# Optimization experiments

Measured on AMD Instinct MI355X. Metric: run time of the kernel, lower is better.

## Reference

```python
import jax, jax.numpy as jnp
import numpy as np

B, T, D, H, HD, I = 256, 1, 2048, 16, 128, 5504
EPS = 1e-6
ROPE_THETA = 10000.0


def setup_inputs() -> dict:
    key = jax.random.key(0)
    ks = jax.random.split(key, 20)
    W = 0.02  # weight init scale
    hidden_states = jax.random.normal(ks[0], (B, T, D), jnp.float32)
    # RoPE tables for each batch element at a distinct decode position
    pos = jnp.arange(B, dtype=jnp.float32) % 4096.0
    inv_freq = 1.0 / (ROPE_THETA ** (jnp.arange(0, HD, 2, dtype=jnp.float32) / HD))
    ang = pos[:, None] * inv_freq[None, :]                      # [B, HD/2]
    emb = jnp.concatenate([ang, ang], axis=-1)                  # [B, HD]
    cos = jnp.cos(emb)[:, None, :]                              # [B, 1, HD]
    sin = jnp.sin(emb)[:, None, :]
    n = lambda k, s: jax.random.normal(k, s, jnp.float32) * W
    return {
        'hidden_states': hidden_states, 'cos': cos, 'sin': sin,
        'router_w': n(ks[1], (D,)), 'router_b': jnp.zeros((1,), jnp.float32),
        'ln1_w': jnp.ones((D,), jnp.float32), 'ln2_w': jnp.ones((D,), jnp.float32),
        'wq': n(ks[2], (D, D)), 'bq': jnp.zeros((D,), jnp.float32),
        'wk': n(ks[3], (D, D)), 'bk': jnp.zeros((D,), jnp.float32),
        'wv': n(ks[4], (D, D)), 'bv': jnp.zeros((D,), jnp.float32),
        'wo': n(ks[5], (D, D)),
        'w_gate': n(ks[6], (D, I)), 'w_up': n(ks[7], (D, I)), 'w_down': n(ks[8], (I, D)),
        'k_sel': 128,
    }


def _rms(x, w):
    v = jnp.mean(jnp.square(x), axis=-1, keepdims=True)
    return x * jax.lax.rsqrt(v + EPS) * w


def _rotate_half(x):
    x1, x2 = jnp.split(x, 2, axis=-1)
    return jnp.concatenate([-x2, x1], axis=-1)


def _decoder_layer(x, cs, sn, ln1_w, ln2_w, wq, bq, wk, bk, wv, bv, wo, w_gate, w_up, w_down):
    # x: [k, T, D]; cs/sn: [k, T, HD]
    k = x.shape[0]
    h = _rms(x, ln1_w)
    q = (h @ wq + bq).reshape(k, T, H, HD).transpose(0, 2, 1, 3)  # [k,H,T,HD]
    kk = (h @ wk + bk).reshape(k, T, H, HD).transpose(0, 2, 1, 3)
    v = (h @ wv + bv).reshape(k, T, H, HD).transpose(0, 2, 1, 3)
    c = cs[:, None, :, :]  # [k,1,T,HD]
    s = sn[:, None, :, :]
    q = q * c + _rotate_half(q) * s
    kk = kk * c + _rotate_half(kk) * s
    att = jnp.einsum('bhqd,bhkd->bhqk', q, kk) * (HD ** -0.5)
    p = jax.nn.softmax(att, axis=-1)  # T==1: trivial causal mask
    o = jnp.einsum('bhqk,bhkd->bhqd', p, v).transpose(0, 2, 1, 3).reshape(k, T, D) @ wo
    x = x + o
    h2 = _rms(x, ln2_w)
    mlp = (jax.nn.silu(h2 @ w_gate) * (h2 @ w_up)) @ w_down
    return x + mlp


def reference(hidden_states, cos, sin, router_w, router_b, ln1_w, ln2_w,
              wq, bq, wk, bk, wv, bv, wo, w_gate, w_up, w_down, k_sel):
    # causal router: linear D->1 scores per batch row (T==1 decode step)
    scores = hidden_states[:, 0, :] @ router_w + router_b[0]   # [B]
    probs = jax.nn.sigmoid(scores)
    _, sel_idx = jax.lax.top_k(probs, k_sel)                   # [k]
    x_sel = hidden_states[sel_idx]                             # gather [k,T,D]
    cs, sn = cos[sel_idx], sin[sel_idx]                        # [k,T,HD]
    x_out = _decoder_layer(x_sel, cs, sn, ln1_w, ln2_w, wq, bq, wk, bk,
                           wv, bv, wo, w_gate, w_up, w_down)
    return hidden_states.at[sel_idx].set(x_out)                # scatter back
```

## Files before the change

### kernel.cpp

```cpp
#include <hip/hip_runtime.h>
#include <hip/hip_bf16.h>
#include <stdint.h>


#define D_ 2048
#define I_ 5504
#define NROWS 256
#define KSEL 128

typedef __attribute__((ext_vector_type(8))) short short8;
typedef __attribute__((ext_vector_type(4))) float floatx4;

__device__ __forceinline__ unsigned short f2bf(float f) {
  union { float f; unsigned int u; } v; v.f = f;
  unsigned int r = (v.u + 0x7FFFu + ((v.u >> 16) & 1u)) >> 16;
  return (unsigned short)r;
}

__device__ __forceinline__ unsigned int pk2(float lo, float hi) {
  __hip_bfloat162 h = __float22bfloat162_rn(float2{lo, hi});
  unsigned int u; __builtin_memcpy(&u, &h, 4); return u;
}

__global__ void k_router(const float* __restrict__ hid, const float* __restrict__ rw,
                         const float* __restrict__ rb, float* __restrict__ scores) {
  int b = blockIdx.x, t = threadIdx.x;
  const float* x = hid + (size_t)b * D_;
  float s = 0.f;
  for (int i = t; i < D_; i += 256) s += x[i] * rw[i];
  for (int o = 32; o; o >>= 1) s += __shfl_down(s, o);
  __shared__ float red[4];
  if ((t & 63) == 0) red[t >> 6] = s;
  __syncthreads();
  if (t == 0) scores[b] = red[0] + red[1] + red[2] + red[3] + rb[0];
}

__global__ void k_select(const float* __restrict__ scores, const int* __restrict__ kptr,
                         int* __restrict__ sel, int* __restrict__ pos) {
  __shared__ float sv[NROWS];
  int t = threadIdx.x;
  sv[t] = scores[t];
  __syncthreads();
  float s = sv[t];
  int c = 0;
  for (int j = 0; j < NROWS; ++j) {
    float o = sv[j];
    c += (o > s) || (o == s && j < t);
  }
  int k = *kptr;
  if (c < k) sel[c] = t;
  pos[t] = (c < k) ? c : -1;
}

__global__ void k_rms1(const float* __restrict__ hid, const int* __restrict__ sel,
                       const float* __restrict__ ln1, const float* __restrict__ bv,
                       unsigned short* __restrict__ Hb, float* __restrict__ V,
                       float* __restrict__ X1) {
  int i = blockIdx.x, t = threadIdx.x;
  int r = sel[i];
  const float* x = hid + (size_t)r * D_;
  float xs[8]; float ss = 0.f;
#pragma unroll
  for (int c = 0; c < 8; ++c) { float v = x[t + c * 256]; xs[c] = v; ss += v * v; }
  for (int o = 32; o; o >>= 1) ss += __shfl_down(ss, o);
  __shared__ float red[4];
  if ((t & 63) == 0) red[t >> 6] = ss;
  __syncthreads();
  float inv = rsqrtf((red[0] + red[1] + red[2] + red[3]) * (1.0f / D_) + 1e-6f);
#pragma unroll
  for (int c = 0; c < 8; ++c) {
    int idx = t + c * 256;
    size_t o_ = (size_t)i * D_ + idx;
    Hb[o_] = f2bf(xs[c] * inv * ln1[idx]);
    V[o_] = bv[idx];
    X1[o_] = xs[c];
  }
}

__global__ void k_rms2(const float* __restrict__ X1, const float* __restrict__ ln2,
                       unsigned short* __restrict__ H2b, float* __restrict__ G,
                       float* __restrict__ U) {
  int i = blockIdx.x, t = threadIdx.x;
  const float* x = X1 + (size_t)i * D_;
  float xs[8]; float ss = 0.f;
#pragma unroll
  for (int c = 0; c < 8; ++c) { float v = x[t + c * 256]; xs[c] = v; ss += v * v; }
  for (int o = 32; o; o >>= 1) ss += __shfl_down(ss, o);
  __shared__ float red[4];
  if ((t & 63) == 0) red[t >> 6] = ss;
  __syncthreads();
  float inv = rsqrtf((red[0] + red[1] + red[2] + red[3]) * (1.0f / D_) + 1e-6f);
#pragma unroll
  for (int c = 0; c < 8; ++c) {
    int idx = t + c * 256;
    H2b[(size_t)i * D_ + idx] = f2bf(xs[c] * inv * ln2[idx]);
  }
  for (int j = t; j < I_; j += 256) {
    G[(size_t)i * I_ + j] = 0.f;
    U[(size_t)i * I_ + j] = 0.f;
  }
}

__global__ void k_silu_out(const float* __restrict__ G, const float* __restrict__ U,
                           unsigned short* __restrict__ Mb,
                           const float* __restrict__ X1, const int* __restrict__ pos,
                           const float* __restrict__ hid, float* __restrict__ out) {
  int tid = blockIdx.x * 256 + threadIdx.x;
  int stride = gridDim.x * 256;
  const int nM = KSEL * I_;
  for (int i = tid; i < nM; i += stride) {
    float g = G[i], u = U[i];
    float m = (g / (1.f + expf(-g))) * u;
    Mb[i] = f2bf(m);
  }
  const int nO4 = NROWS * (D_ / 4);
  const float4* X14 = (const float4*)X1;
  const float4* H4 = (const float4*)hid;
  float4* O4 = (float4*)out;
  for (int i = tid; i < nO4; i += stride) {
    int row = i >> 9;
    int c4 = i & 511;
    int p = pos[row];
    O4[i] = (p >= 0) ? X14[(size_t)p * 512 + c4] : H4[i];
  }
}

template<bool AF32, bool DUAL>
__global__ __launch_bounds__(256, 2)
void k_gemm(const void* __restrict__ Ap, const float* __restrict__ B0,
            const float* __restrict__ B1, float* __restrict__ C0,
            float* __restrict__ C1, const int* __restrict__ rowmap,
            int K, int KA, int Kb, int lda, int N, int KT, int ldc) {
  constexpr int ST = 72;
  const int bn = blockIdx.x;
  const int kt0 = blockIdx.y * KT;
  const int kt1 = kt0 + KT;
  const int tid = threadIdx.x;
  const int lane = tid & 63;
  const int wave = tid >> 6;
  const int wm = wave >> 1, wn = wave & 1;
  const int fm = lane & 15, kq = lane >> 4;

  __shared__ alignas(16) unsigned short Asm[128 * ST];
  __shared__ alignas(16) unsigned short Bsm0[32 * ST];
  __shared__ alignas(16) unsigned short Bsm1[DUAL ? 32 * ST : 8];

  floatx4 acc0[4] = {};
  floatx4 acc1[4] = {};

  const int ar = tid >> 1;
  const int ah = (tid & 1) * 32;
  const int bnn = tid & 31;
  const int bk8 = (tid >> 5) * 8;

  const unsigned short* Ab = AF32 ? nullptr : (const unsigned short*)Ap + (size_t)ar * lda + ah;
  const float*          Af = AF32 ? (const float*)Ap + (size_t)ar * lda + ah : nullptr;
  const float* B0c = B0 + (size_t)(bn * 32 + bnn);
  const float* B1c = DUAL ? B1 + (size_t)(bn * 32 + bnn) : nullptr;

  uint4 a4[4];
  float4 af8[8];
  float b0v[8], b1v[8];

  auto load_tile = [&](int kt) {
    if (AF32) {
#pragma unroll
      for (int r = 0; r < 8; ++r) {
        int c0 = kt + ah + r * 4;
        af8[r] = (c0 < KA) ? *(const float4*)(Af + kt + r * 4)
                           : make_float4(0.f, 0.f, 0.f, 0.f);
      }
    } else {
#pragma unroll
      for (int r = 0; r < 4; ++r) {
        int c0 = kt + ah + r * 8;
        a4[r] = (c0 < KA) ? *(const uint4*)(Ab + kt + r * 8)
                          : make_uint4(0u, 0u, 0u, 0u);
      }
    }
#pragma unroll
    for (int j = 0; j < 8; ++j) {
      int kr = kt + bk8 + j; kr = kr < Kb ? kr : Kb - 1;
      b0v[j] = B0c[(size_t)kr * N];
      if (DUAL) b1v[j] = B1c[(size_t)kr * N];
    }
  };

  load_tile(kt0);

  for (int kt = kt0; kt < kt1; kt += 64) {
    __syncthreads();
    {
      uint4* Ad = (uint4*)&Asm[ar * ST + ah];
      if (AF32) {
        uint4 q;
#pragma unroll
        for (int r = 0; r < 4; ++r) {
          q.x = pk2(af8[2 * r].x, af8[2 * r].y);
          q.y = pk2(af8[2 * r].z, af8[2 * r].w);
          q.z = pk2(af8[2 * r + 1].x, af8[2 * r + 1].y);
          q.w = pk2(af8[2 * r + 1].z, af8[2 * r + 1].w);
          Ad[r] = q;
        }
      } else {
#pragma unroll
        for (int r = 0; r < 4; ++r) Ad[r] = a4[r];
      }
      uint4 bq;
      bq.x = pk2(b0v[0], b0v[1]); bq.y = pk2(b0v[2], b0v[3]);
      bq.z = pk2(b0v[4], b0v[5]); bq.w = pk2(b0v[6], b0v[7]);
      *(uint4*)&Bsm0[bnn * ST + bk8] = bq;
      if (DUAL) {
        uint4 cq;
        cq.x = pk2(b1v[0], b1v[1]); cq.y = pk2(b1v[2], b1v[3]);
        cq.z = pk2(b1v[4], b1v[5]); cq.w = pk2(b1v[6], b1v[7]);
        *(uint4*)&Bsm1[bnn * ST + bk8] = cq;
      }
    }
    __syncthreads();
    if (kt + 64 < kt1) load_tile(kt + 64);
    short8 afr[2][4], bf0[2], bf1[2];
#pragma unroll
    for (int s = 0; s < 2; ++s) {
#pragma unroll
      for (int i = 0; i < 4; ++i)
        afr[s][i] = *(const short8*)&Asm[(wm * 64 + i * 16 + fm) * ST + s * 32 + kq * 8];
      bf0[s] = *(const short8*)&Bsm0[(wn * 16 + fm) * ST + s * 32 + kq * 8];
      if (DUAL)
        bf1[s] = *(const short8*)&Bsm1[(wn * 16 + fm) * ST + s * 32 + kq * 8];
    }
#pragma unroll
    for (int s = 0; s < 2; ++s) {
#pragma unroll
      for (int i = 0; i < 4; ++i) {
        acc0[i] = __builtin_amdgcn_mfma_f32_16x16x32_bf16(afr[s][i], bf0[s], acc0[i], 0, 0, 0);
        if (DUAL)
          acc1[i] = __builtin_amdgcn_mfma_f32_16x16x32_bf16(afr[s][i], bf1[s], acc1[i], 0, 0, 0);
      }
    }
  }

#pragma unroll
  for (int i = 0; i < 4; ++i) {
#pragma unroll
    for (int r = 0; r < 4; ++r) {
      int row = wm * 64 + i * 16 + kq * 4 + r;
      size_t rbase = rowmap ? (size_t)rowmap[row] * ldc : (size_t)row * ldc;
      int col = bn * 32 + wn * 16 + fm;
      atomicAdd(&C0[rbase + col], acc0[i][r]);
      if (DUAL) atomicAdd(&C1[rbase + col], acc1[i][r]);
    }
  }
}

extern "C" void kernel_launch(void* const* d_in, const int* in_sizes, int n_in,
                              void* d_out, int out_size, void* d_ws, size_t ws_size,
                              hipStream_t stream) {
  const float* hid = (const float*)d_in[0];
  const float* rw  = (const float*)d_in[3];
  const float* rb  = (const float*)d_in[4];
  const float* ln1 = (const float*)d_in[5];
  const float* ln2 = (const float*)d_in[6];
  const float* wv  = (const float*)d_in[11];
  const float* bv  = (const float*)d_in[12];
  const float* wo  = (const float*)d_in[13];
  const float* wg  = (const float*)d_in[14];
  const float* wu  = (const float*)d_in[15];
  const float* wd  = (const float*)d_in[16];
  const int*   kp  = (const int*)d_in[17];
  float* out = (float*)d_out;

  char* ws = (char*)d_ws;
  float*          scores = (float*)(ws + 0);
  int*            sel    = (int*)(ws + 1024);
  int*            pos    = (int*)(ws + 1536);
  unsigned short* Hb     = (unsigned short*)(ws + 4096);
  float*          V      = (float*)(ws + 528384);
  float*          X1     = (float*)(ws + 1576960);
  unsigned short* H2b    = (unsigned short*)(ws + 2625536);
  float*          G      = (float*)(ws + 3149824);
  float*          U      = (float*)(ws + 5967872);
  unsigned short* Mb     = (unsigned short*)(ws + 8785920);

  k_router<<<256, 256, 0, stream>>>(hid, rw, rb, scores);
  k_select<<<1, 256, 0, stream>>>(scores, kp, sel, pos);
  k_rms1<<<128, 256, 0, stream>>>(hid, sel, ln1, bv, Hb, V, X1);
  k_gemm<false, false><<<dim3(64, 8), 256, 0, stream>>>(
      Hb, wv, nullptr, V, nullptr, nullptr, 2048, 2048, 2048, 2048, 2048, 256, 2048);
  k_gemm<true, false><<<dim3(64, 8), 256, 0, stream>>>(
      V, wo, nullptr, X1, nullptr, nullptr, 2048, 2048, 2048, 2048, 2048, 256, 2048);
  k_rms2<<<128, 256, 0, stream>>>(X1, ln2, H2b, G, U);
  k_gemm<false, true><<<dim3(172, 4), 256, 0, stream>>>(
      H2b, wg, wu, G, U, nullptr, 2048, 2048, 2048, 2048, 5504, 512, 5504);
  k_silu_out<<<1024, 256, 0, stream>>>(G, U, Mb, X1, pos, hid, out);
  k_gemm<false, false><<<dim3(64, 8), 256, 0, stream>>>(
      Mb, wd, nullptr, out, nullptr, sel, 5632, 5504, 5504, 5504, 2048, 704, 2048);
}
```

Before: 295.1 us.

## Drop LDS staging in split-K GEMM, load MFMA fragments directly into registers

```diff
diff --git a/kernel.cpp b/kernel.cpp
--- a/kernel.cpp
+++ b/kernel.cpp
@@ -126,12 +126,11 @@
 }
 
 template<bool AF32, bool DUAL>
-__global__ __launch_bounds__(256, 2)
+__global__ __launch_bounds__(256)
 void k_gemm(const void* __restrict__ Ap, const float* __restrict__ B0,
             const float* __restrict__ B1, float* __restrict__ C0,
             float* __restrict__ C1, const int* __restrict__ rowmap,
             int K, int KA, int Kb, int lda, int N, int KT, int ldc) {
-  constexpr int ST = 72;
   const int bn = blockIdx.x;
   const int kt0 = blockIdx.y * KT;
   const int kt1 = kt0 + KT;
@@ -141,104 +140,81 @@
   const int wm = wave >> 1, wn = wave & 1;
   const int fm = lane & 15, kq = lane >> 4;
 
-  __shared__ alignas(16) unsigned short Asm[128 * ST];
-  __shared__ alignas(16) unsigned short Bsm0[32 * ST];
-  __shared__ alignas(16) unsigned short Bsm1[DUAL ? 32 * ST : 8];
-
   floatx4 acc0[4] = {};
   floatx4 acc1[4] = {};
 
-  const int ar = tid >> 1;
-  const int ah = (tid & 1) * 32;
-  const int bnn = tid & 31;
-  const int bk8 = (tid >> 5) * 8;
-
-  const unsigned short* Ab = AF32 ? nullptr : (const unsigned short*)Ap + (size_t)ar * lda + ah;
-  const float*          Af = AF32 ? (const float*)Ap + (size_t)ar * lda + ah : nullptr;
-  const float* B0c = B0 + (size_t)(bn * 32 + bnn);
-  const float* B1c = DUAL ? B1 + (size_t)(bn * 32 + bnn) : nullptr;
-
-  uint4 a4[4];
-  float4 af8[8];
-  float b0v[8], b1v[8];
-
-  auto load_tile = [&](int kt) {
+  const unsigned short* Ab_lane = AF32 ? nullptr
+      : (const unsigned short*)Ap + (size_t)(wm * 64 + fm) * lda + kq * 8;
+  const float* Af_lane = AF32
+      ? (const float*)Ap + (size_t)(wm * 64 + fm) * lda + kq * 8 : nullptr;
+  const float* B0c = B0 + (size_t)(bn * 32 + wn * 16 + fm);
+  const float* B1c = DUAL ? B1 + (size_t)(bn * 32 + wn * 16 + fm) : nullptr;
+
+  short8 aR[2][4];
+  float4 aF[2][8];
+  float  bR0[2][8], bR1[2][8];
+
+  auto loadStep = [&](int bk, int kt) {
     if (AF32) {
 #pragma unroll
-      for (int r = 0; r < 8; ++r) {
-        int c0 = kt + ah + r * 4;
-        af8[r] = (c0 < KA) ? *(const float4*)(Af + kt + r * 4)
-                           : make_float4(0.f, 0.f, 0.f, 0.f);
+      for (int i = 0; i < 4; ++i) {
+        const float* ap = Af_lane + (size_t)i * 16 * lda + kt;
+        aF[bk][2 * i]     = *(const float4*)ap;
+        aF[bk][2 * i + 1] = *(const float4*)(ap + 4);
       }
     } else {
 #pragma unroll
-      for (int r = 0; r < 4; ++r) {
-        int c0 = kt + ah + r * 8;
-        a4[r] = (c0 < KA) ? *(const uint4*)(Ab + kt + r * 8)
-                          : make_uint4(0u, 0u, 0u, 0u);
+      for (int i = 0; i < 4; ++i) {
+        aR[bk][i] = short8{};
+        if (kt + kq * 8 < KA)
+          aR[bk][i] = *(const short8*)(Ab_lane + (size_t)i * 16 * lda + kt);
       }
     }
 #pragma unroll
     for (int j = 0; j < 8; ++j) {
-      int kr = kt + bk8 + j; kr = kr < Kb ? kr : Kb - 1;
-      b0v[j] = B0c[(size_t)kr * N];
-      if (DUAL) b1v[j] = B1c[(size_t)kr * N];
+      int kr = kt + kq * 8 + j; kr = kr < Kb ? kr : Kb - 1;
+      bR0[bk][j] = B0c[(size_t)kr * N];
+      if (DUAL) bR1[bk][j] = B1c[(size_t)kr * N];
     }
   };
 
-  load_tile(kt0);
-
-  for (int kt = kt0; kt < kt1; kt += 64) {
-    __syncthreads();
-    {
-      uint4* Ad = (uint4*)&Asm[ar * ST + ah];
+  auto computeStep = [&](int bk) {
+    union { short8 s; unsigned int u[4]; } b0, b1;
+    b0.u[0] = pk2(bR0[bk][0], bR0[bk][1]); b0.u[1] = pk2(bR0[bk][2], bR0[bk][3]);
+    b0.u[2] = pk2(bR0[bk][4], bR0[bk][5]); b0.u[3] = pk2(bR0[bk][6], bR0[bk][7]);
+    if (DUAL) {
+      b1.u[0] = pk2(bR1[bk][0], bR1[bk][1]); b1.u[1] = pk2(bR1[bk][2], bR1[bk][3]);
+      b1.u[2] = pk2(bR1[bk][4], bR1[bk][5]); b1.u[3] = pk2(bR1[bk][6], bR1[bk][7]);
+    }
+#pragma unroll
+    for (int i = 0; i < 4; ++i) {
+      short8 a;
       if (AF32) {
-        uint4 q;
-#pragma unroll
-        for (int r = 0; r < 4; ++r) {
-          q.x = pk2(af8[2 * r].x, af8[2 * r].y);
-          q.y = pk2(af8[2 * r].z, af8[2 * r].w);
-          q.z = pk2(af8[2 * r + 1].x, af8[2 * r + 1].y);
-          q.w = pk2(af8[2 * r + 1].z, af8[2 * r + 1].w);
-          Ad[r] = q;
-        }
+        union { short8 s; unsigned int u[4]; } p;
+        float4 x0 = aF[bk][2 * i], x1 = aF[bk][2 * i + 1];
+        p.u[0] = pk2(x0.x, x0.y); p.u[1] = pk2(x0.z, x0.w);
+        p.u[2] = pk2(x1.x, x1.y); p.u[3] = pk2(x1.z, x1.w);
+        a = p.s;
       } else {
-#pragma unroll
-        for (int r = 0; r < 4; ++r) Ad[r] = a4[r];
+        a = aR[bk][i];
       }
-      uint4 bq;
-      bq.x = pk2(b0v[0], b0v[1]); bq.y = pk2(b0v[2], b0v[3]);
-      bq.z = pk2(b0v[4], b0v[5]); bq.w = pk2(b0v[6], b0v[7]);
-      *(uint4*)&Bsm0[bnn * ST + bk8] = bq;
-      if (DUAL) {
-        uint4 cq;
-        cq.x = pk2(b1v[0], b1v[1]); cq.y = pk2(b1v[2], b1v[3]);
-        cq.z = pk2(b1v[4], b1v[5]); cq.w = pk2(b1v[6], b1v[7]);
-        *(uint4*)&Bsm1[bnn * ST + bk8] = cq;
-      }
-    }
-    __syncthreads();
-    if (kt + 64 < kt1) load_tile(kt + 64);
-    short8 afr[2][4], bf0[2], bf1[2];
-#pragma unroll
-    for (int s = 0; s < 2; ++s) {
-#pragma unroll
-      for (int i = 0; i < 4; ++i)
-        afr[s][i] = *(const short8*)&Asm[(wm * 64 + i * 16 + fm) * ST + s * 32 + kq * 8];
-      bf0[s] = *(const short8*)&Bsm0[(wn * 16 + fm) * ST + s * 32 + kq * 8];
+      acc0[i] = __builtin_amdgcn_mfma_f32_16x16x32_bf16(a, b0.s, acc0[i], 0, 0, 0);
       if (DUAL)
-        bf1[s] = *(const short8*)&Bsm1[(wn * 16 + fm) * ST + s * 32 + kq * 8];
-    }
-#pragma unroll
-    for (int s = 0; s < 2; ++s) {
-#pragma unroll
-      for (int i = 0; i < 4; ++i) {
-        acc0[i] = __builtin_amdgcn_mfma_f32_16x16x32_bf16(afr[s][i], bf0[s], acc0[i], 0, 0, 0);
-        if (DUAL)
-          acc1[i] = __builtin_amdgcn_mfma_f32_16x16x32_bf16(afr[s][i], bf1[s], acc1[i], 0, 0, 0);
-      }
-    }
-  }
+        acc1[i] = __builtin_amdgcn_mfma_f32_16x16x32_bf16(a, b1.s, acc1[i], 0, 0, 0);
+    }
+  };
+
+  loadStep(0, kt0);
+  int kt = kt0;
+  for (; kt + 64 < kt1; kt += 64) {
+    loadStep(1, kt + 32);
+    computeStep(0);
+    loadStep(0, kt + 64);
+    computeStep(1);
+  }
+  loadStep(1, kt + 32);
+  computeStep(0);
+  computeStep(1);
 
 #pragma unroll
   for (int i = 0; i < 4; ++i) {
```

Measured after the change: 353.8 us. 19.9% more time.
